# Performance work log

Hardware: AMD Instinct MI355X
Metric: run time of the kernel (lower is better)

Reference implementation:

```python
import jax, jax.numpy as jnp
import numpy as np

EMBED = 4096
HEADS = 64
HEAD_DIM = EMBED // HEADS  # 64
BATCH = 256
SEQ = HEADS  # forced equal by the module's final reshape


def setup_inputs() -> dict:
    key = jax.random.key(0)
    k1, k2, k3, k4, k5 = jax.random.split(key, 5)
    values = jax.random.normal(k1, (BATCH, SEQ, EMBED), dtype=jnp.float32)
    keys = jax.random.normal(k2, (BATCH, SEQ, EMBED), dtype=jnp.float32)
    query = jax.random.normal(k3, (BATCH, SEQ, EMBED), dtype=jnp.float32)
    mask = jax.random.randint(k4, (BATCH, SEQ), 0, 2, dtype=jnp.int32)
    w_out = jax.random.normal(k5, (EMBED, EMBED), dtype=jnp.float32) * 0.02
    b_out = jnp.zeros((EMBED,), dtype=jnp.float32)
    return {"values": values, "keys": keys, "query": query, "mask": mask,
            "w_out": w_out, "b_out": b_out}


def reference(values, keys, query, mask, w_out, b_out):
    # NOTE: faithful to the original module, including its quirks:
    #  - the qkv Linear layers are defined but never applied in forward
    #  - the einsum labels the HEAD axis as q/k and the SEQ axis as h
    N, Lq, E = query.shape
    H, D = HEADS, HEAD_DIM
    v = values.reshape(N, -1, H, D).transpose(2, 0, 1, 3)   # (H, N, L, D)
    k = keys.reshape(N, -1, H, D).transpose(2, 0, 1, 3)     # (H, N, L, D)
    q = query.reshape(N, Lq, H, D).transpose(2, 0, 1, 3)    # (H, N, L, D)
    # energy: (q=H, k=H, n=N, h=L) contracted over d
    energy = jnp.einsum('qnhd,knhd->qknh', q, k)
    energy = jnp.where(mask == 0, jnp.float32(-1e20), energy)  # mask (N,L) broadcasts
    attention = jax.nn.softmax(energy / jnp.sqrt(jnp.float32(D)), axis=2)
    # out: (q=H, k=H, n=N, d=D), summed over v(=H) and h(=L)
    out = jnp.einsum('qknh,vnhd->qknd', attention, v)
    out = out.transpose(1, 2, 0, 3).reshape(N, Lq, H * D)  # valid since H == Lq
    return out @ w_out.T + b_out
```

## Files before the change

### kernel.cpp

```cpp
#include <hip/hip_runtime.h>

typedef __attribute__((ext_vector_type(4))) float floatx4;
typedef __attribute__((ext_vector_type(8))) short short8;


__device__ __forceinline__ unsigned short f2bf(float x) {
    union { float f; unsigned u; } v; v.f = x;
    unsigned r = v.u + 0x7FFFu + ((v.u >> 16) & 1u);
    return (unsigned short)(r >> 16);
}
__device__ __forceinline__ float bf2f(unsigned short h) {
    union { unsigned u; float f; } v; v.u = ((unsigned)h) << 16; return v.f;
}
__device__ __forceinline__ unsigned pk2(float a, float b) {
    return (unsigned)f2bf(a) | ((unsigned)f2bf(b) << 16);
}

__global__ void cast_w(const float* __restrict__ w, unsigned short* __restrict__ wb) {
    size_t i = ((size_t)blockIdx.x * 256 + threadIdx.x) * 4;
    float4 v = *(const float4*)(w + i);
    ushort4 o;
    o.x = f2bf(v.x); o.y = f2bf(v.y); o.z = f2bf(v.z); o.w = f2bf(v.w);
    *(ushort4*)(wb + i) = o;
}

__global__ void vsum_k(const float* __restrict__ values, float* __restrict__ vsum) {
    const int t = threadIdx.x;
    const int d = t & 63;
    const int nh = blockIdx.x * 4 + (t >> 6);
    const float* base = values + (size_t)nh * 4096 + d;
    float acc = 0.f;
    #pragma unroll
    for (int vh = 0; vh < 64; vh++) acc += base[vh * 64];
    vsum[(size_t)nh * 64 + d] = acc;
}

#define QS 68
__global__ __launch_bounds__(256) void energy_k(const float* __restrict__ query,
        const float* __restrict__ keys, const int* __restrict__ mask,
        unsigned short* __restrict__ P, float* __restrict__ denom) {
    __shared__ __align__(16) float QsT[64 * QS];
    __shared__ __align__(16) float KsT[64 * QS];
    const int h = blockIdx.y;
    const int nc = blockIdx.x;
    const int t = threadIdx.x;
    const int qg = t >> 4;
    const int kg = t & 15;
    float dacc[16];
    #pragma unroll
    for (int i = 0; i < 16; i++) dacc[i] = 0.f;
    unsigned* Pu = (unsigned*)P;

    for (int n = nc * 16; n < nc * 16 + 16; n++) {
        if (mask[n * 64 + h] == 0) {
            const size_t b32 = (size_t)n * 131072 + (size_t)h * 32;
            #pragma unroll
            for (int i = 0; i < 8; i++) {
                int idx2 = i * 256 + t;
                Pu[b32 + (size_t)(idx2 >> 5) * 2048 + (idx2 & 31)] = 0u;
            }
            continue;
        }
        const float* qsrc = query + ((size_t)n * 64 + h) * 4096;
        const float* ksrc = keys + ((size_t)n * 64 + h) * 4096;
        __syncthreads();
        #pragma unroll
        for (int i = 0; i < 4; i++) {
            int v = i * 256 + t;
            int row = v >> 4;
            int d0 = (v & 15) * 4;
            float4 q4 = *(const float4*)(qsrc + (size_t)v * 4);
            float4 k4 = *(const float4*)(ksrc + (size_t)v * 4);
            QsT[(d0 + 0) * QS + row] = q4.x;
            QsT[(d0 + 1) * QS + row] = q4.y;
            QsT[(d0 + 2) * QS + row] = q4.z;
            QsT[(d0 + 3) * QS + row] = q4.w;
            KsT[(d0 + 0) * QS + row] = k4.x;
            KsT[(d0 + 1) * QS + row] = k4.y;
            KsT[(d0 + 2) * QS + row] = k4.z;
            KsT[(d0 + 3) * QS + row] = k4.w;
        }
        __syncthreads();
        float e[16];
        #pragma unroll
        for (int i = 0; i < 16; i++) e[i] = 0.f;
        #pragma unroll 8
        for (int d = 0; d < 64; d++) {
            floatx4 qv = *(const floatx4*)(QsT + d * QS + qg * 4);
            floatx4 kv = *(const floatx4*)(KsT + d * QS + kg * 4);
            e[0]  += qv.x * kv.x; e[1]  += qv.x * kv.y; e[2]  += qv.x * kv.z; e[3]  += qv.x * kv.w;
            e[4]  += qv.y * kv.x; e[5]  += qv.y * kv.y; e[6]  += qv.y * kv.z; e[7]  += qv.y * kv.w;
            e[8]  += qv.z * kv.x; e[9]  += qv.z * kv.y; e[10] += qv.z * kv.z; e[11] += qv.z * kv.w;
            e[12] += qv.w * kv.x; e[13] += qv.w * kv.y; e[14] += qv.w * kv.z; e[15] += qv.w * kv.w;
        }
        const size_t pbase = (size_t)n * 262144 + (size_t)h * 64 + qg * 4;
        #pragma unroll
        for (int b = 0; b < 4; b++) {
            float p0 = __expf(e[0 * 4 + b] * 0.125f);
            float p1 = __expf(e[1 * 4 + b] * 0.125f);
            float p2 = __expf(e[2 * 4 + b] * 0.125f);
            float p3 = __expf(e[3 * 4 + b] * 0.125f);
            dacc[0 * 4 + b] += p0; dacc[1 * 4 + b] += p1;
            dacc[2 * 4 + b] += p2; dacc[3 * 4 + b] += p3;
            ushort4 s;
            s.x = f2bf(p0); s.y = f2bf(p1); s.z = f2bf(p2); s.w = f2bf(p3);
            *(ushort4*)(P + pbase + (size_t)(kg * 4 + b) * 4096) = s;
        }
    }
    #pragma unroll
    for (int a = 0; a < 4; a++)
        #pragma unroll
        for (int b = 0; b < 4; b++)
            atomicAdd(denom + ((size_t)(kg * 4 + b) * 64 + h) * 64 + qg * 4 + a,
                      dacc[a * 4 + b]);
}

#define VSD 68
__global__ __launch_bounds__(256) void pv_k(const unsigned short* P_in,
        const float* __restrict__ denom, const float* __restrict__ vsum,
        unsigned short* F) {
    __shared__ __align__(16) unsigned short attn[4 * 64 * 64];
    __shared__ __align__(16) float Vs[64 * VSD];
    const int kg4 = blockIdx.x;
    const int n = blockIdx.y;
    const int t = threadIdx.x;
    #pragma unroll
    for (int i = 0; i < 4; i++) {
        int v = i * 256 + t;
        float4 x = *(const float4*)(vsum + (size_t)n * 4096 + (size_t)v * 4);
        int hh = v >> 4, d0 = (v & 15) * 4;
        *(float4*)(Vs + hh * VSD + d0) = x;
    }
    const size_t slice = ((size_t)n * 64 + kg4 * 4) * 4096;
    const uint4* Pv = (const uint4*)(P_in + slice);
    const float* dsl = denom + (size_t)kg4 * 4 * 4096;
    uint4* Av = (uint4*)attn;
    #pragma unroll
    for (int i = 0; i < 8; i++) {
        int j = i * 256 + t;
        uint4 raw = Pv[j];
        floatx4 d0 = *(const floatx4*)(dsl + (size_t)j * 8);
        floatx4 d1 = *(const floatx4*)(dsl + (size_t)j * 8 + 4);
        float v0 = bf2f((unsigned short)(raw.x & 0xffff)) * __builtin_amdgcn_rcpf(d0.x);
        float v1 = bf2f((unsigned short)(raw.x >> 16))    * __builtin_amdgcn_rcpf(d0.y);
        float v2 = bf2f((unsigned short)(raw.y & 0xffff)) * __builtin_amdgcn_rcpf(d0.z);
        float v3 = bf2f((unsigned short)(raw.y >> 16))    * __builtin_amdgcn_rcpf(d0.w);
        float v4 = bf2f((unsigned short)(raw.z & 0xffff)) * __builtin_amdgcn_rcpf(d1.x);
        float v5 = bf2f((unsigned short)(raw.z >> 16))    * __builtin_amdgcn_rcpf(d1.y);
        float v6 = bf2f((unsigned short)(raw.w & 0xffff)) * __builtin_amdgcn_rcpf(d1.z);
        float v7 = bf2f((unsigned short)(raw.w >> 16))    * __builtin_amdgcn_rcpf(d1.w);
        uint4 o;
        o.x = pk2(v0, v1); o.y = pk2(v2, v3); o.z = pk2(v4, v5); o.w = pk2(v6, v7);
        Av[j] = o;
    }
    __syncthreads();
    const int qq = t >> 2, dsub = t & 3;
    floatx4 acc[4][4];
    #pragma unroll
    for (int b = 0; b < 4; b++)
        #pragma unroll
        for (int m = 0; m < 4; m++) acc[b][m] = (floatx4)(0.f);
    #pragma unroll 4
    for (int h = 0; h < 64; h++) {
        float a0 = bf2f(attn[(0 * 64 + h) * 64 + qq]);
        float a1 = bf2f(attn[(1 * 64 + h) * 64 + qq]);
        float a2 = bf2f(attn[(2 * 64 + h) * 64 + qq]);
        float a3 = bf2f(attn[(3 * 64 + h) * 64 + qq]);
        floatx4 w0 = *(const floatx4*)(Vs + h * VSD + dsub * 16);
        floatx4 w1 = *(const floatx4*)(Vs + h * VSD + dsub * 16 + 4);
        floatx4 w2 = *(const floatx4*)(Vs + h * VSD + dsub * 16 + 8);
        floatx4 w3 = *(const floatx4*)(Vs + h * VSD + dsub * 16 + 12);
        acc[0][0] += a0 * w0; acc[0][1] += a0 * w1; acc[0][2] += a0 * w2; acc[0][3] += a0 * w3;
        acc[1][0] += a1 * w0; acc[1][1] += a1 * w1; acc[1][2] += a1 * w2; acc[1][3] += a1 * w3;
        acc[2][0] += a2 * w0; acc[2][1] += a2 * w1; acc[2][2] += a2 * w2; acc[2][3] += a2 * w3;
        acc[3][0] += a3 * w0; acc[3][1] += a3 * w1; acc[3][2] += a3 * w2; acc[3][3] += a3 * w3;
    }
    #pragma unroll
    for (int b = 0; b < 4; b++) {
        size_t base = ((size_t)n * 64 + kg4 * 4 + b) * 4096 + qq * 64 + dsub * 16;
        uint4 o0, o1;
        o0.x = pk2(acc[b][0].x, acc[b][0].y); o0.y = pk2(acc[b][0].z, acc[b][0].w);
        o0.z = pk2(acc[b][1].x, acc[b][1].y); o0.w = pk2(acc[b][1].z, acc[b][1].w);
        o1.x = pk2(acc[b][2].x, acc[b][2].y); o1.y = pk2(acc[b][2].z, acc[b][2].w);
        o1.z = pk2(acc[b][3].x, acc[b][3].y); o1.w = pk2(acc[b][3].z, acc[b][3].w);
        *(uint4*)(F + base) = o0;
        *(uint4*)(F + base + 8) = o1;
    }
}

__device__ __forceinline__ void gload_lds16(const unsigned short* g, unsigned short* lds) {
    __builtin_amdgcn_global_load_lds(
        (const __attribute__((address_space(1))) unsigned int*)g,
        (__attribute__((address_space(3))) unsigned int*)lds, 16, 0, 0);
}

__global__ __launch_bounds__(256) void gemm_bt(const unsigned short* __restrict__ A,
        const unsigned short* __restrict__ B, const float* __restrict__ bias,
        float* __restrict__ C) {
    __shared__ __align__(16) unsigned short As[128 * 32];
    __shared__ __align__(16) unsigned short Bs[128 * 32];
    const int t = threadIdx.x;
    const int w = t >> 6, l = t & 63;
    const int m0 = blockIdx.y * 128;
    const int n0 = blockIdx.x * 128;
    const int c0 = w * 64 + l;
    const int c1 = c0 + 256;
    const int rA0 = c0 >> 2, o0 = (c0 & 3) * 8;
    const int rA1 = c1 >> 2, o1 = (c1 & 3) * 8;
    const unsigned short* gA0 = A + (size_t)(m0 + rA0) * 4096 + o0;
    const unsigned short* gA1 = A + (size_t)(m0 + rA1) * 4096 + o1;
    const unsigned short* gB0 = B + (size_t)(n0 + rA0) * 4096 + o0;
    const unsigned short* gB1 = B + (size_t)(n0 + rA1) * 4096 + o1;
    unsigned short* lA0 = As + w * 512;
    unsigned short* lA1 = As + 2048 + w * 512;
    unsigned short* lB0 = Bs + w * 512;
    unsigned short* lB1 = Bs + 2048 + w * 512;
    const int wr = w >> 1, wc = w & 1, r16 = l & 15, quad = l >> 4;
    floatx4 acc[4][4];
    #pragma unroll
    for (int mi = 0; mi < 4; mi++)
        #pragma unroll
        for (int ni = 0; ni < 4; ni++) acc[mi][ni] = (floatx4)(0.f);

    for (int kb = 0; kb < 128; kb++) {
        const int k0 = kb * 32;
        gload_lds16(gA0 + k0, lA0);
        gload_lds16(gA1 + k0, lA1);
        gload_lds16(gB0 + k0, lB0);
        gload_lds16(gB1 + k0, lB1);
        __syncthreads();
        short8 af[4], bf[4];
        #pragma unroll
        for (int mi = 0; mi < 4; mi++)
            af[mi] = *(const short8*)(As + (wr * 64 + mi * 16 + r16) * 32 + quad * 8);
        #pragma unroll
        for (int ni = 0; ni < 4; ni++)
            bf[ni] = *(const short8*)(Bs + (wc * 64 + ni * 16 + r16) * 32 + quad * 8);
        #pragma unroll
        for (int mi = 0; mi < 4; mi++)
            #pragma unroll
            for (int ni = 0; ni < 4; ni++)
                acc[mi][ni] = __builtin_amdgcn_mfma_f32_16x16x32_bf16(
                    af[mi], bf[ni], acc[mi][ni], 0, 0, 0);
        __syncthreads();
    }
    #pragma unroll
    for (int mi = 0; mi < 4; mi++) {
        #pragma unroll
        for (int ni = 0; ni < 4; ni++) {
            const int col = n0 + wc * 64 + ni * 16 + r16;
            const float bv = bias[col];
            #pragma unroll
            for (int r = 0; r < 4; r++) {
                const int rp = m0 + wr * 64 + mi * 16 + quad * 4 + r;
                const int crow = ((rp & 63) << 8) | (rp >> 6);
                C[(size_t)crow * 4096 + col] = acc[mi][ni][r] + bv;
            }
        }
    }
}

extern "C" void kernel_launch(void* const* d_in, const int* in_sizes, int n_in,
                              void* d_out, int out_size, void* d_ws, size_t ws_size,
                              hipStream_t stream) {
    const float* values = (const float*)d_in[0];
    const float* keys   = (const float*)d_in[1];
    const float* query  = (const float*)d_in[2];
    const int*   mask   = (const int*)d_in[3];
    const float* w_out  = (const float*)d_in[4];
    const float* b_out  = (const float*)d_in[5];
    float* out = (float*)d_out;

    char* ws = (char*)d_ws;
    unsigned short* P  = (unsigned short*)ws;
    unsigned short* wb = (unsigned short*)(ws + 134217728);
    float* vsum        = (float*)(ws + 167772160);
    float* denom       = (float*)(ws + 171966464);

    hipMemsetAsync(denom, 0, 262144 * sizeof(float), stream);
    cast_w<<<16384, 256, 0, stream>>>(w_out, wb);
    vsum_k<<<4096, 256, 0, stream>>>(values, vsum);
    energy_k<<<dim3(16, 64), 256, 0, stream>>>(query, keys, mask, P, denom);
    pv_k<<<dim3(16, 256), 256, 0, stream>>>(P, denom, vsum, P);
    gemm_bt<<<dim3(32, 128), 256, 0, stream>>>(P, wb, b_out, out);
}
```

Measured before the change: 1.537 ms.

## Compute energy with bf16 MFMA and move denominator sum to separate kernel

Replaces the FP32 scalar-FMA energy kernel with one that converts Q/K rows to bf16 in registers and uses 16x16x32 bf16 MFMA. Exponentiated results are staged in shared memory and written to P with coalesced 16-byte stores. The per-thread atomic denominator accumulation is dropped in favour of a separate denom_k pass that re-reads P, which also removes the memset. This trades extra precision loss in QK (bf16 inputs) and an extra read of the 128MB P buffer for far faster energy compute and no atomics.

Measured after the change: 1.499 ms. 2.4% less time.

```diff
diff --git a/kernel.cpp b/kernel.cpp
--- a/kernel.cpp
+++ b/kernel.cpp
@@ -35,84 +35,111 @@
     vsum[(size_t)nh * 64 + d] = acc;
 }
 
-#define QS 68
-__global__ __launch_bounds__(256) void energy_k(const float* __restrict__ query,
+union U16 { uint4 u; short8 s; };
+
+__global__ __launch_bounds__(256) void energy_k2(const float* __restrict__ query,
         const float* __restrict__ keys, const int* __restrict__ mask,
-        unsigned short* __restrict__ P, float* __restrict__ denom) {
-    __shared__ __align__(16) float QsT[64 * QS];
-    __shared__ __align__(16) float KsT[64 * QS];
-    const int h = blockIdx.y;
-    const int nc = blockIdx.x;
+        unsigned short* __restrict__ P) {
+    __shared__ __align__(16) unsigned short T[64 * 256];
+    const int n = blockIdx.y;
+    const int hq = blockIdx.x;
     const int t = threadIdx.x;
-    const int qg = t >> 4;
-    const int kg = t & 15;
-    float dacc[16];
-    #pragma unroll
-    for (int i = 0; i < 16; i++) dacc[i] = 0.f;
-    unsigned* Pu = (unsigned*)P;
-
-    for (int n = nc * 16; n < nc * 16 + 16; n++) {
-        if (mask[n * 64 + h] == 0) {
-            const size_t b32 = (size_t)n * 131072 + (size_t)h * 32;
-            #pragma unroll
-            for (int i = 0; i < 8; i++) {
-                int idx2 = i * 256 + t;
-                Pu[b32 + (size_t)(idx2 >> 5) * 2048 + (idx2 & 31)] = 0u;
+    const int w = t >> 6, l = t & 63;
+    const int r16 = l & 15, quad = l >> 4;
+    const int kw = w >> 1, qw = w & 1;
+    unsigned short* Pn = P + (size_t)n * 262144;
+
+    for (int hc = 0; hc < 4; hc++) {
+        const int h0 = hq * 16 + hc * 4;
+        for (int h4 = 0; h4 < 4; h4++) {
+            const int h = h0 + h4;
+            if (mask[n * 64 + h] == 0) {
+                #pragma unroll
+                for (int mi = 0; mi < 2; mi++)
+                    #pragma unroll
+                    for (int ni = 0; ni < 2; ni++)
+                        #pragma unroll
+                        for (int r = 0; r < 4; r++)
+                            T[(kw*32 + mi*16 + quad*4 + r) * 256 + h4*64
+                              + qw*32 + ni*16 + r16] = 0;
+                continue;
             }
-            continue;
-        }
-        const float* qsrc = query + ((size_t)n * 64 + h) * 4096;
-        const float* ksrc = keys + ((size_t)n * 64 + h) * 4096;
-        __syncthreads();
-        #pragma unroll
-        for (int i = 0; i < 4; i++) {
-            int v = i * 256 + t;
-            int row = v >> 4;
-            int d0 = (v & 15) * 4;
-            float4 q4 = *(const float4*)(qsrc + (size_t)v * 4);
-            float4 k4 = *(const float4*)(ksrc + (size_t)v * 4);
-            QsT[(d0 + 0) * QS + row] = q4.x;
-            QsT[(d0 + 1) * QS + row] = q4.y;
-            QsT[(d0 + 2) * QS + row] = q4.z;
-            QsT[(d0 + 3) * QS + row] = q4.w;
-            KsT[(d0 + 0) * QS + row] = k4.x;
-            KsT[(d0 + 1) * QS + row] = k4.y;
-            KsT[(d0 + 2) * QS + row] = k4.z;
-            KsT[(d0 + 3) * QS + row] = k4.w;
+            const float* Qr = query + ((size_t)n * 64 + h) * 4096;
+            const float* Kr = keys  + ((size_t)n * 64 + h) * 4096;
+            short8 af[2][2], bf[2][2];
+            #pragma unroll
+            for (int mi = 0; mi < 2; mi++)
+                #pragma unroll
+                for (int ks = 0; ks < 2; ks++) {
+                    const float* src = Kr + (kw*32 + mi*16 + r16) * 64 + ks*32 + quad*8;
+                    float4 x = *(const float4*)src;
+                    float4 y = *(const float4*)(src + 4);
+                    U16 u; u.u.x = pk2(x.x, x.y); u.u.y = pk2(x.z, x.w);
+                    u.u.z = pk2(y.x, y.y); u.u.w = pk2(y.z, y.w);
+                    af[mi][ks] = u.s;
+                }
+            #pragma unroll
+            for (int ni = 0; ni < 2; ni++)
+                #pragma unroll
+                for (int ks = 0; ks < 2; ks++) {
+                    const float* src = Qr + (qw*32 + ni*16 + r16) * 64 + ks*32 + quad*8;
+                    float4 x = *(const float4*)src;
+                    float4 y = *(const float4*)(src + 4);
+                    U16 u; u.u.x = pk2(x.x, x.y); u.u.y = pk2(x.z, x.w);
+                    u.u.z = pk2(y.x, y.y); u.u.w = pk2(y.z, y.w);
+                    bf[ni][ks] = u.s;
+                }
+            floatx4 acc[2][2];
+            #pragma unroll
+            for (int mi = 0; mi < 2; mi++)
+                #pragma unroll
+                for (int ni = 0; ni < 2; ni++) acc[mi][ni] = (floatx4)(0.f);
+            #pragma unroll
+            for (int ks = 0; ks < 2; ks++)
+                #pragma unroll
+                for (int mi = 0; mi < 2; mi++)
+                    #pragma unroll
+                    for (int ni = 0; ni < 2; ni++)
+                        acc[mi][ni] = __builtin_amdgcn_mfma_f32_16x16x32_bf16(
+                            af[mi][ks], bf[ni][ks], acc[mi][ni], 0, 0, 0);
+            #pragma unroll
+            for (int mi = 0; mi < 2; mi++)
+                #pragma unroll
+                for (int ni = 0; ni < 2; ni++)
+                    #pragma unroll
+                    for (int r = 0; r < 4; r++) {
+                        float p = __expf(acc[mi][ni][r] * 0.125f);
+                        T[(kw*32 + mi*16 + quad*4 + r) * 256 + h4*64
+                          + qw*32 + ni*16 + r16] = f2bf(p);
+                    }
         }
         __syncthreads();
-        float e[16];
-        #pragma unroll
-        for (int i = 0; i < 16; i++) e[i] = 0.f;
-        #pragma unroll 8
-        for (int d = 0; d < 64; d++) {
-            floatx4 qv = *(const floatx4*)(QsT + d * QS + qg * 4);
-            floatx4 kv = *(const floatx4*)(KsT + d * QS + kg * 4);
-            e[0]  += qv.x * kv.x; e[1]  += qv.x * kv.y; e[2]  += qv.x * kv.z; e[3]  += qv.x * kv.w;
-            e[4]  += qv.y * kv.x; e[5]  += qv.y * kv.y; e[6]  += qv.y * kv.z; e[7]  += qv.y * kv.w;
-            e[8]  += qv.z * kv.x; e[9]  += qv.z * kv.y; e[10] += qv.z * kv.z; e[11] += qv.z * kv.w;
-            e[12] += qv.w * kv.x; e[13] += qv.w * kv.y; e[14] += qv.w * kv.z; e[15] += qv.w * kv.w;
+        #pragma unroll
+        for (int i = 0; i < 8; i++) {
+            int s = i * 256 + t;
+            int k = s >> 5, u = s & 31;
+            uint4 v = ((const uint4*)T)[s];
+            *(uint4*)(Pn + (size_t)k * 4096 + h0 * 64 + u * 8) = v;
         }
-        const size_t pbase = (size_t)n * 262144 + (size_t)h * 64 + qg * 4;
-        #pragma unroll
-        for (int b = 0; b < 4; b++) {
-            float p0 = __expf(e[0 * 4 + b] * 0.125f);
-            float p1 = __expf(e[1 * 4 + b] * 0.125f);
-            float p2 = __expf(e[2 * 4 + b] * 0.125f);
-            float p3 = __expf(e[3 * 4 + b] * 0.125f);
-            dacc[0 * 4 + b] += p0; dacc[1 * 4 + b] += p1;
-            dacc[2 * 4 + b] += p2; dacc[3 * 4 + b] += p3;
-            ushort4 s;
-            s.x = f2bf(p0); s.y = f2bf(p1); s.z = f2bf(p2); s.w = f2bf(p3);
-            *(ushort4*)(P + pbase + (size_t)(kg * 4 + b) * 4096) = s;
-        }
-    }
-    #pragma unroll
-    for (int a = 0; a < 4; a++)
-        #pragma unroll
-        for (int b = 0; b < 4; b++)
-            atomicAdd(denom + ((size_t)(kg * 4 + b) * 64 + h) * 64 + qg * 4 + a,
-                      dacc[a * 4 + b]);
+        __syncthreads();
+    }
+}
+
+__global__ __launch_bounds__(256) void denom_k(const unsigned short* __restrict__ P,
+        float* __restrict__ denom) {
+    const int j0 = (blockIdx.x * 256 + threadIdx.x) * 4;
+    const unsigned short* p = P + j0;
+    float s0 = 0.f, s1 = 0.f, s2 = 0.f, s3 = 0.f;
+    #pragma unroll 8
+    for (int n = 0; n < 256; n++) {
+        uint2 v = *(const uint2*)(p + (size_t)n * 262144);
+        s0 += bf2f((unsigned short)(v.x & 0xffff));
+        s1 += bf2f((unsigned short)(v.x >> 16));
+        s2 += bf2f((unsigned short)(v.y & 0xffff));
+        s3 += bf2f((unsigned short)(v.y >> 16));
+    }
+    float4 o; o.x = s0; o.y = s1; o.z = s2; o.w = s3;
+    *(float4*)(denom + j0) = o;
 }
 
 #define VSD 68
@@ -277,10 +304,10 @@
     float* vsum        = (float*)(ws + 167772160);
     float* denom       = (float*)(ws + 171966464);
 
-    hipMemsetAsync(denom, 0, 262144 * sizeof(float), stream);
     cast_w<<<16384, 256, 0, stream>>>(w_out, wb);
     vsum_k<<<4096, 256, 0, stream>>>(values, vsum);
-    energy_k<<<dim3(16, 64), 256, 0, stream>>>(query, keys, mask, P, denom);
+    energy_k2<<<dim3(4, 256), 256, 0, stream>>>(query, keys, mask, P);
+    denom_k<<<256, 256, 0, stream>>>(P, denom);
     pv_k<<<dim3(16, 256), 256, 0, stream>>>(P, denom, vsum, P);
     gemm_bt<<<dim3(32, 128), 256, 0, stream>>>(P, wb, b_out, out);
 }
```
